# Performance work log

Measured on AMD Instinct MI355X. Metric: run time of the kernel, lower is better.

Reference implementation:

```python
import jax, jax.numpy as jnp
import numpy as np

NUM_EXPERT = 16
IN_FEAT = 1024
OUT_FEAT = 1024
BATCH = 8192


def setup_inputs() -> dict:
    key = jax.random.key(0)
    k_inp, k_gate, k_w = jax.random.split(key, 3)
    inp = jax.random.normal(k_inp, (BATCH, IN_FEAT), dtype=jnp.float32)
    gate = jax.random.randint(k_gate, (BATCH,), 0, NUM_EXPERT, dtype=jnp.int32)
    # nn.Linear default init: uniform(-1/sqrt(in_feat), 1/sqrt(in_feat))
    bound = 1.0 / np.sqrt(IN_FEAT)
    weight = jax.random.uniform(
        k_w, (NUM_EXPERT, OUT_FEAT, IN_FEAT), dtype=jnp.float32,
        minval=-bound, maxval=bound)
    return {"inp": inp, "gate": gate, "weight": weight}


def reference(inp, gate, weight):
    # o[t] = weight[gate[t]] @ inp[t]
    # Loop over the (small, fixed) expert axis via lax.scan; each step does a
    # dense [B, in] @ [in, out] GEMM and keeps rows routed to that expert.
    num_expert, out_feat, _ = weight.shape
    batch = inp.shape[0]

    def body(o, xs):
        i, w = xs  # w: [out_feat, in_feat]
        y = inp @ w.T  # [batch, out_feat]
        sel = (gate == i)[:, None]
        return jnp.where(sel, y, o), None

    o0 = jnp.zeros((batch, out_feat), dtype=inp.dtype)
    o, _ = jax.lax.scan(body, o0, (jnp.arange(num_expert), weight))
    return o
```

## Files before the change

### kernel.cpp

```cpp
#include <hip/hip_runtime.h>
#include <hip/hip_bf16.h>

#define NE    16
#define KDIM  1024
#define NDIM  1024
#define BATCH 8192
#define TM    128
#define TN    64
#define MAXT  96

typedef __attribute__((ext_vector_type(8))) short short8;
typedef __attribute__((ext_vector_type(4))) float floatx4;
typedef unsigned short ushort_t;

#define O_TG0  1024
#define O_TE   2048
#define O_TEND 3072
#define O_GIDX 4096
#define O_TOK  36864
#define O_PA   73728
#define WS_REQ 17113088

#define GLOAD_LDS(gp, lp) __builtin_amdgcn_global_load_lds( \
    (const __attribute__((address_space(1))) unsigned int*)(gp), \
    (__attribute__((address_space(3))) unsigned int*)(lp), 16, 0, 0)

__device__ __forceinline__ unsigned int pk2bf(float x, float y) {
    __hip_bfloat162 h = __float22bfloat162_rn(make_float2(x, y));
    unsigned int u;
    __builtin_memcpy(&u, &h, 4);
    return u;
}


__global__ __launch_bounds__(1024) void map_k(
        const int* __restrict__ gate, int* __restrict__ gidx,
        int* __restrict__ tg0, int* __restrict__ te, int* __restrict__ tend) {
    __shared__ int ccnt[128][NE];
    __shared__ int cbase[128][NE];
    __shared__ int ebase[NE];
    __shared__ int etot[NE];
    const int tid = threadIdx.x;
    const int wv = tid >> 6, ln = tid & 63;

    ((int*)ccnt)[tid] = 0;
    ((int*)ccnt)[tid + 1024] = 0;
    __syncthreads();

    int e[8], rk[8];
    #pragma unroll
    for (int i = 0; i < 8; ++i) {
        const int chunk = wv * 8 + i;
        const int t = chunk * 64 + ln;
        const int ei = gate[t];
        unsigned long long m = ~0ull;
        #pragma unroll
        for (int b = 0; b < 4; ++b) {
            unsigned long long bb = __ballot(((ei >> b) & 1) != 0);
            m &= ((ei >> b) & 1) ? bb : ~bb;
        }
        const unsigned int lo = (unsigned int)m;
        const unsigned int hi = (unsigned int)(m >> 32);
        const int r = __builtin_amdgcn_mbcnt_hi(
            hi, __builtin_amdgcn_mbcnt_lo(lo, 0));
        if (r == 0) ccnt[chunk][ei] = __popcll(m);
        e[i] = ei; rk[i] = r;
    }
    __syncthreads();

    if (tid < NE) {
        int s = 0;
        for (int c = 0; c < 128; ++c) { cbase[c][tid] = s; s += ccnt[c][tid]; }
        etot[tid] = s;
    }
    __syncthreads();

    if (tid == 0) {
        int o = 0, nt = 0;
        for (int j = 0; j < NE; ++j) {
            ebase[j] = o;
            int c = etot[j];
            for (int rr = 0; rr < c; rr += TM) {
                int r0 = (rr + TM <= c) ? rr : (c > TM ? c - TM : 0);
                tg0[nt] = o + r0; te[nt] = j; tend[nt] = o + c; ++nt;
            }
            o += c;
        }
        for (; nt < MAXT; ++nt) { tg0[nt] = 0; te[nt] = 0; tend[nt] = 0; }
    }
    __syncthreads();

    #pragma unroll
    for (int i = 0; i < 8; ++i) {
        const int chunk = wv * 8 + i;
        const int t = chunk * 64 + ln;
        gidx[t] = ebase[e[i]] + cbase[chunk][e[i]] + rk[i];
    }
}

__global__ __launch_bounds__(256, 8) void gather_k(
        const float* __restrict__ inp, const int* __restrict__ gidx,
        ushort_t* __restrict__ pA, int* __restrict__ tok) {
    const int b = blockIdx.x, tid = threadIdx.x;
    const int col = (tid & 127) * 8;
    const int half = tid >> 7;
    int g[2]; float4 v0[2], v1[2];
    #pragma unroll
    for (int p = 0; p < 2; ++p) {
        int t = b * 4 + p * 2 + half;
        g[p] = gidx[t];
        v0[p] = *(const float4*)&inp[(size_t)t * KDIM + col];
        v1[p] = *(const float4*)&inp[(size_t)t * KDIM + col + 4];
    }
    #pragma unroll
    for (int p = 0; p < 2; ++p) {
        uint4 u = make_uint4(pk2bf(v0[p].x, v0[p].y), pk2bf(v0[p].z, v0[p].w),
                             pk2bf(v1[p].x, v1[p].y), pk2bf(v1[p].z, v1[p].w));
        *(uint4*)&pA[(size_t)g[p] * KDIM + col] = u;
        if (col == 0) tok[g[p]] = b * 4 + p * 2 + half;
    }
}

__global__ __launch_bounds__(256, 5) void moe_gemm5_k(
        const ushort_t* __restrict__ pA, const float* __restrict__ wgt,
        const int* __restrict__ tg0, const int* __restrict__ teArr,
        const int* __restrict__ tend, const int* __restrict__ tok,
        float* __restrict__ out) {
    const int id  = blockIdx.x;
    const int y   = (id & 7) + 8 * (id >> 7);
    const int xb  = (id >> 3) & 15;
    const int g0  = tg0[y];
    const int end = tend[y];
    if (g0 >= end) return;
    const int e    = teArr[y];
    const int out0 = xb * TN;

    __shared__ ushort_t As[TM][64];
    __shared__ ushort_t Bs[TN][64];
    __shared__ int tok_s[TM];

    const int tid = threadIdx.x;
    if (tid < TM) tok_s[tid] = tok[g0 + tid];

    const int wave = tid >> 6, lane = tid & 63;
    const int wm = (wave >> 1) * 64;
    const int wn = (wave & 1) * 32;
    const int quad = lane >> 4, l16 = lane & 15;

    const ushort_t* Ab = pA + (size_t)g0 * KDIM;
    const float*    Bw = wgt + ((size_t)e * NDIM + out0) * KDIM;

    floatx4 acc[4][2] = {};
    const int slotw = wave * 64 + lane;

    for (int k0 = 0; k0 < KDIM; k0 += 64) {
        float4 bv[2][2];
        #pragma unroll
        for (int i = 0; i < 2; ++i) {
            int slot = i * 256 + slotw;
            int row = slot >> 3;
            int kc = (slot & 7) ^ (row & 7);
            const float* src = Bw + (size_t)row * KDIM + k0 + kc * 8;
            bv[i][0] = *(const float4*)src;
            bv[i][1] = *(const float4*)(src + 4);
        }
        #pragma unroll
        for (int i = 0; i < 4; ++i) {
            int slot = i * 256 + slotw;
            int row = slot >> 3;
            int kc = (slot & 7) ^ (row & 7);
            GLOAD_LDS(Ab + (size_t)row * KDIM + k0 + kc * 8,
                      (ushort_t*)As + (size_t)(i * 256 + wave * 64) * 8);
        }
        #pragma unroll
        for (int i = 0; i < 2; ++i) {
            int slot = i * 256 + slotw;
            uint4 u = make_uint4(pk2bf(bv[i][0].x, bv[i][0].y),
                                 pk2bf(bv[i][0].z, bv[i][0].w),
                                 pk2bf(bv[i][1].x, bv[i][1].y),
                                 pk2bf(bv[i][1].z, bv[i][1].w));
            *(uint4*)((ushort_t*)Bs + (size_t)slot * 8) = u;
        }
        __syncthreads();
        #pragma unroll
        for (int s = 0; s < 2; ++s) {
            short8 a[4], b[2];
            #pragma unroll
            for (int i = 0; i < 4; ++i) {
                int r = wm + i * 16 + l16;
                a[i] = *(const short8*)&As[r][((s * 4 + quad) ^ (r & 7)) * 8];
            }
            #pragma unroll
            for (int j = 0; j < 2; ++j) {
                int r = wn + j * 16 + l16;
                b[j] = *(const short8*)&Bs[r][((s * 4 + quad) ^ (r & 7)) * 8];
            }
            #pragma unroll
            for (int mi = 0; mi < 4; ++mi)
                #pragma unroll
                for (int nj = 0; nj < 2; ++nj)
                    acc[mi][nj] = __builtin_amdgcn_mfma_f32_16x16x32_bf16(
                        a[mi], b[nj], acc[mi][nj], 0, 0, 0);
        }
        __syncthreads();
    }

    #pragma unroll
    for (int mi = 0; mi < 4; ++mi) {
        #pragma unroll
        for (int r = 0; r < 4; ++r) {
            int lrow = wm + mi * 16 + quad * 4 + r;
            if (g0 + lrow < end) {
                int t = tok_s[lrow];
                float* orow = out + (size_t)t * NDIM + out0 + wn + l16;
                #pragma unroll
                for (int nj = 0; nj < 2; ++nj)
                    orow[nj * 16] = acc[mi][nj][r];
            }
        }
    }
}

#define LDW 20
__global__ void zero_k(int* cnt) {
    if (threadIdx.x < NE) cnt[threadIdx.x] = 0;
}

__global__ void bin_tokens_k(const int* __restrict__ gate, int* cnt, int* idx) {
    int t = blockIdx.x * blockDim.x + threadIdx.x;
    if (t < BATCH) {
        int e = gate[t];
        int p = atomicAdd(&cnt[e], 1);
        idx[e * BATCH + p] = t;
    }
}

__global__ __launch_bounds__(256) void moe_gemm_k(
        const float* __restrict__ inp, const float* __restrict__ wgt,
        const int* __restrict__ cnt, const int* __restrict__ idx,
        float* __restrict__ out) {
    const int e = blockIdx.z;
    const int n_e = cnt[e];
    const int row0 = blockIdx.y * TM;
    if (row0 >= n_e) return;
    const int out0 = blockIdx.x * 128;
    __shared__ unsigned int As[TM * LDW];
    __shared__ unsigned int Bs[TM * LDW];
    __shared__ int tok_s[TM];
    const int tid = threadIdx.x;
    if (tid < TM) {
        int g = row0 + tid;
        tok_s[tid] = (g < n_e) ? idx[e * BATCH + g] : -1;
    }
    const int wave = tid >> 6, lane = tid & 63;
    const int wm = (wave >> 1) * 64, wn = (wave & 1) * 64;
    const int quad = lane >> 4, l16 = lane & 15;
    floatx4 acc[4][4] = {};
    const int cg = (tid & 7) * 4;
    const int rbase = tid >> 3;
    const float* wbase = wgt + (size_t)e * KDIM * NDIM;
    for (int k0 = 0; k0 < KDIM; k0 += 32) {
        __syncthreads();
        #pragma unroll
        for (int p = 0; p < 4; ++p) {
            int row = p * 32 + rbase;
            int t = tok_s[row];
            float4 va = make_float4(0.f, 0.f, 0.f, 0.f);
            if (t >= 0) va = *(const float4*)&inp[(size_t)t * KDIM + k0 + cg];
            As[row * LDW + (cg >> 1)]     = pk2bf(va.x, va.y);
            As[row * LDW + (cg >> 1) + 1] = pk2bf(va.z, va.w);
            float4 vb = *(const float4*)&wbase[(size_t)(out0 + row) * KDIM + k0 + cg];
            Bs[row * LDW + (cg >> 1)]     = pk2bf(vb.x, vb.y);
            Bs[row * LDW + (cg >> 1) + 1] = pk2bf(vb.z, vb.w);
        }
        __syncthreads();
        short8 a[4], b[4];
        #pragma unroll
        for (int i = 0; i < 4; ++i)
            a[i] = *(const short8*)&As[(wm + i * 16 + l16) * LDW + quad * 4];
        #pragma unroll
        for (int i = 0; i < 4; ++i)
            b[i] = *(const short8*)&Bs[(wn + i * 16 + l16) * LDW + quad * 4];
        #pragma unroll
        for (int mi = 0; mi < 4; ++mi)
            #pragma unroll
            for (int ni = 0; ni < 4; ++ni)
                acc[mi][ni] = __builtin_amdgcn_mfma_f32_16x16x32_bf16(
                    a[mi], b[ni], acc[mi][ni], 0, 0, 0);
    }
    #pragma unroll
    for (int mi = 0; mi < 4; ++mi) {
        #pragma unroll
        for (int r = 0; r < 4; ++r) {
            int lrow = wm + mi * 16 + quad * 4 + r;
            int t = tok_s[lrow];
            if (t >= 0) {
                float* orow = out + (size_t)t * NDIM + out0 + wn + l16;
                #pragma unroll
                for (int ni = 0; ni < 4; ++ni)
                    orow[ni * 16] = acc[mi][ni][r];
            }
        }
    }
}

extern "C" void kernel_launch(void* const* d_in, const int* in_sizes, int n_in,
                              void* d_out, int out_size, void* d_ws, size_t ws_size,
                              hipStream_t stream) {
    const float* inp  = (const float*)d_in[0];
    const int*   gate = (const int*)d_in[1];
    const float* wgt  = (const float*)d_in[2];
    float*       out  = (float*)d_out;
    char* w = (char*)d_ws;

    if (ws_size >= WS_REQ) {
        int* tg0  = (int*)(w + O_TG0);
        int* te   = (int*)(w + O_TE);
        int* tend = (int*)(w + O_TEND);
        int* gidx = (int*)(w + O_GIDX);
        int* tok  = (int*)(w + O_TOK);
        ushort_t* pA = (ushort_t*)(w + O_PA);

        map_k<<<1, 1024, 0, stream>>>(gate, gidx, tg0, te, tend);
        gather_k<<<2048, 256, 0, stream>>>(inp, gidx, pA, tok);
        moe_gemm5_k<<<16 * MAXT, 256, 0, stream>>>(pA, wgt, tg0, te, tend, tok, out);
    } else {
        int* cnt = (int*)d_ws;
        int* idx = cnt + NE;
        zero_k<<<1, 64, 0, stream>>>(cnt);
        bin_tokens_k<<<BATCH / 256, 256, 0, stream>>>(gate, cnt, idx);
        dim3 grid(NDIM / 128, BATCH / TM, NE);
        moe_gemm_k<<<grid, 256, 0, stream>>>(inp, wgt, cnt, idx, out);
    }
}
```

Baseline: 180.3 us.

## Fuse token gather and bf16 conversion into the grouped GEMM A-tile load

Drops the separate gather kernel that wrote a permuted bf16 copy of the input. The GEMM now reads fp32 input rows directly through the token index list, converts them to bf16 in registers and stores them to LDS. This saves one kernel launch and a full write and read of the permuted activations. In exchange, each A tile is converted again by every one of the 16 output-column blocks, A traffic is doubled in fp32, and the LDS-direct async loads are gone. The launch also changes to a plain 2D grid without the block-id swizzle, and occupancy drops from 5 to 4 blocks.

```diff
diff --git a/kernel.cpp b/kernel.cpp
--- a/kernel.cpp
+++ b/kernel.cpp
@@ -16,14 +16,8 @@
 #define O_TG0  1024
 #define O_TE   2048
 #define O_TEND 3072
-#define O_GIDX 4096
 #define O_TOK  36864
-#define O_PA   73728
 #define WS_REQ 17113088
-
-#define GLOAD_LDS(gp, lp) __builtin_amdgcn_global_load_lds( \
-    (const __attribute__((address_space(1))) unsigned int*)(gp), \
-    (__attribute__((address_space(3))) unsigned int*)(lp), 16, 0, 0)
 
 __device__ __forceinline__ unsigned int pk2bf(float x, float y) {
     __hip_bfloat162 h = __float22bfloat162_rn(make_float2(x, y));
@@ -34,7 +28,7 @@
 
 
 __global__ __launch_bounds__(1024) void map_k(
-        const int* __restrict__ gate, int* __restrict__ gidx,
+        const int* __restrict__ gate, int* __restrict__ tok,
         int* __restrict__ tg0, int* __restrict__ te, int* __restrict__ tend) {
     __shared__ int ccnt[128][NE];
     __shared__ int cbase[128][NE];
@@ -94,46 +88,22 @@
     for (int i = 0; i < 8; ++i) {
         const int chunk = wv * 8 + i;
         const int t = chunk * 64 + ln;
-        gidx[t] = ebase[e[i]] + cbase[chunk][e[i]] + rk[i];
-    }
-}
-
-__global__ __launch_bounds__(256, 8) void gather_k(
-        const float* __restrict__ inp, const int* __restrict__ gidx,
-        ushort_t* __restrict__ pA, int* __restrict__ tok) {
-    const int b = blockIdx.x, tid = threadIdx.x;
-    const int col = (tid & 127) * 8;
-    const int half = tid >> 7;
-    int g[2]; float4 v0[2], v1[2];
-    #pragma unroll
-    for (int p = 0; p < 2; ++p) {
-        int t = b * 4 + p * 2 + half;
-        g[p] = gidx[t];
-        v0[p] = *(const float4*)&inp[(size_t)t * KDIM + col];
-        v1[p] = *(const float4*)&inp[(size_t)t * KDIM + col + 4];
-    }
-    #pragma unroll
-    for (int p = 0; p < 2; ++p) {
-        uint4 u = make_uint4(pk2bf(v0[p].x, v0[p].y), pk2bf(v0[p].z, v0[p].w),
-                             pk2bf(v1[p].x, v1[p].y), pk2bf(v1[p].z, v1[p].w));
-        *(uint4*)&pA[(size_t)g[p] * KDIM + col] = u;
-        if (col == 0) tok[g[p]] = b * 4 + p * 2 + half;
-    }
-}
-
-__global__ __launch_bounds__(256, 5) void moe_gemm5_k(
-        const ushort_t* __restrict__ pA, const float* __restrict__ wgt,
+        tok[ebase[e[i]] + cbase[chunk][e[i]] + rk[i]] = t;
+    }
+    if (tid < TM) tok[BATCH + tid] = 0;
+}
+
+__global__ __launch_bounds__(256, 4) void moe_gemm6_k(
+        const float* __restrict__ inp, const float* __restrict__ wgt,
         const int* __restrict__ tg0, const int* __restrict__ teArr,
         const int* __restrict__ tend, const int* __restrict__ tok,
         float* __restrict__ out) {
-    const int id  = blockIdx.x;
-    const int y   = (id & 7) + 8 * (id >> 7);
-    const int xb  = (id >> 3) & 15;
+    const int y   = blockIdx.y;
     const int g0  = tg0[y];
     const int end = tend[y];
     if (g0 >= end) return;
     const int e    = teArr[y];
-    const int out0 = xb * TN;
+    const int out0 = blockIdx.x * TN;
 
     __shared__ ushort_t As[TM][64];
     __shared__ ushort_t Bs[TN][64];
@@ -147,39 +117,51 @@
     const int wn = (wave & 1) * 32;
     const int quad = lane >> 4, l16 = lane & 15;
 
-    const ushort_t* Ab = pA + (size_t)g0 * KDIM;
-    const float*    Bw = wgt + ((size_t)e * NDIM + out0) * KDIM;
+    const int rbase = tid >> 3;
+    const int dcol  = (tid & 7) * 8;
+    const int kc    = ((tid & 7) ^ (rbase & 7)) * 8;
+
+    __syncthreads();
+
+    const float* arow[4];
+    #pragma unroll
+    for (int i = 0; i < 4; ++i)
+        arow[i] = inp + (size_t)tok_s[rbase + 32 * i] * KDIM + kc;
+    const float* Bw = wgt + ((size_t)e * NDIM + out0) * KDIM;
+    const float* brow[2];
+    #pragma unroll
+    for (int i = 0; i < 2; ++i)
+        brow[i] = Bw + (size_t)(rbase + 32 * i) * KDIM + kc;
 
     floatx4 acc[4][2] = {};
-    const int slotw = wave * 64 + lane;
 
     for (int k0 = 0; k0 < KDIM; k0 += 64) {
-        float4 bv[2][2];
+        float4 av[4][2], bv[2][2];
+        #pragma unroll
+        for (int i = 0; i < 4; ++i) {
+            av[i][0] = *(const float4*)(arow[i] + k0);
+            av[i][1] = *(const float4*)(arow[i] + k0 + 4);
+        }
         #pragma unroll
         for (int i = 0; i < 2; ++i) {
-            int slot = i * 256 + slotw;
-            int row = slot >> 3;
-            int kc = (slot & 7) ^ (row & 7);
-            const float* src = Bw + (size_t)row * KDIM + k0 + kc * 8;
-            bv[i][0] = *(const float4*)src;
-            bv[i][1] = *(const float4*)(src + 4);
+            bv[i][0] = *(const float4*)(brow[i] + k0);
+            bv[i][1] = *(const float4*)(brow[i] + k0 + 4);
         }
         #pragma unroll
         for (int i = 0; i < 4; ++i) {
-            int slot = i * 256 + slotw;
-            int row = slot >> 3;
-            int kc = (slot & 7) ^ (row & 7);
-            GLOAD_LDS(Ab + (size_t)row * KDIM + k0 + kc * 8,
-                      (ushort_t*)As + (size_t)(i * 256 + wave * 64) * 8);
+            uint4 u = make_uint4(pk2bf(av[i][0].x, av[i][0].y),
+                                 pk2bf(av[i][0].z, av[i][0].w),
+                                 pk2bf(av[i][1].x, av[i][1].y),
+                                 pk2bf(av[i][1].z, av[i][1].w));
+            *(uint4*)&As[rbase + 32 * i][dcol] = u;
         }
         #pragma unroll
         for (int i = 0; i < 2; ++i) {
-            int slot = i * 256 + slotw;
             uint4 u = make_uint4(pk2bf(bv[i][0].x, bv[i][0].y),
                                  pk2bf(bv[i][0].z, bv[i][0].w),
                                  pk2bf(bv[i][1].x, bv[i][1].y),
                                  pk2bf(bv[i][1].z, bv[i][1].w));
-            *(uint4*)((ushort_t*)Bs + (size_t)slot * 8) = u;
+            *(uint4*)&Bs[rbase + 32 * i][dcol] = u;
         }
         __syncthreads();
         #pragma unroll
@@ -317,13 +299,11 @@
         int* tg0  = (int*)(w + O_TG0);
         int* te   = (int*)(w + O_TE);
         int* tend = (int*)(w + O_TEND);
-        int* gidx = (int*)(w + O_GIDX);
         int* tok  = (int*)(w + O_TOK);
-        ushort_t* pA = (ushort_t*)(w + O_PA);
-
-        map_k<<<1, 1024, 0, stream>>>(gate, gidx, tg0, te, tend);
-        gather_k<<<2048, 256, 0, stream>>>(inp, gidx, pA, tok);
-        moe_gemm5_k<<<16 * MAXT, 256, 0, stream>>>(pA, wgt, tg0, te, tend, tok, out);
+
+        map_k<<<1, 1024, 0, stream>>>(gate, tok, tg0, te, tend);
+        dim3 grid(NDIM / TN, MAXT, 1);
+        moe_gemm6_k<<<grid, 256, 0, stream>>>(inp, wgt, tg0, te, tend, tok, out);
     } else {
         int* cnt = (int*)d_ws;
         int* idx = cnt + NE;
```

Measured after the change: 209.4 us. +16.1%, slower.

## Register-prefetch next K tile in MoE GEMM, replace LDS-direct A loads

Applied to the files above, without the earlier changes.

The grouped GEMM now loads the next K-slice of A and B into registers right after the barrier, so global latency overlaps with the MFMA work on the current slice. The A loads change from global_load_lds to ordinary register loads followed by LDS stores. The trailing barrier becomes a manual lgkmcnt wait plus s_barrier so outstanding vector-memory prefetches are not drained. The grid changes from a 1D swizzled mapping to a plain 2D grid, and occupancy hints drop from 5 to 4 blocks per CU, since holding the prefetch in registers raises register pressure and may reduce occupancy and L2 locality.

```diff
diff --git a/kernel.cpp b/kernel.cpp
--- a/kernel.cpp
+++ b/kernel.cpp
@@ -20,10 +20,6 @@
 #define O_TOK  36864
 #define O_PA   73728
 #define WS_REQ 17113088
-
-#define GLOAD_LDS(gp, lp) __builtin_amdgcn_global_load_lds( \
-    (const __attribute__((address_space(1))) unsigned int*)(gp), \
-    (__attribute__((address_space(3))) unsigned int*)(lp), 16, 0, 0)
 
 __device__ __forceinline__ unsigned int pk2bf(float x, float y) {
     __hip_bfloat162 h = __float22bfloat162_rn(make_float2(x, y));
@@ -121,19 +117,17 @@
     }
 }
 
-__global__ __launch_bounds__(256, 5) void moe_gemm5_k(
+__global__ __launch_bounds__(256, 4) void moe_gemm8_k(
         const ushort_t* __restrict__ pA, const float* __restrict__ wgt,
         const int* __restrict__ tg0, const int* __restrict__ teArr,
         const int* __restrict__ tend, const int* __restrict__ tok,
         float* __restrict__ out) {
-    const int id  = blockIdx.x;
-    const int y   = (id & 7) + 8 * (id >> 7);
-    const int xb  = (id >> 3) & 15;
+    const int y   = blockIdx.y;
     const int g0  = tg0[y];
     const int end = tend[y];
     if (g0 >= end) return;
     const int e    = teArr[y];
-    const int out0 = xb * TN;
+    const int out0 = blockIdx.x * TN;
 
     __shared__ ushort_t As[TM][64];
     __shared__ ushort_t Bs[TN][64];
@@ -146,35 +140,45 @@
     const int wm = (wave >> 1) * 64;
     const int wn = (wave & 1) * 32;
     const int quad = lane >> 4, l16 = lane & 15;
+    const int c8 = tid & 7;
+    const int rb = tid >> 3;
 
     const ushort_t* Ab = pA + (size_t)g0 * KDIM;
     const float*    Bw = wgt + ((size_t)e * NDIM + out0) * KDIM;
 
+    const ushort_t* asrc[4];
+    #pragma unroll
+    for (int i = 0; i < 4; ++i) {
+        int row = rb + 32 * i;
+        asrc[i] = Ab + (size_t)row * KDIM + (c8 ^ (row & 7)) * 8;
+    }
+    const float* bsrc[2];
+    #pragma unroll
+    for (int i = 0; i < 2; ++i) {
+        int slot = i * 256 + tid;
+        int row = slot >> 3;
+        bsrc[i] = Bw + (size_t)row * KDIM + ((slot & 7) ^ (row & 7)) * 8;
+    }
+
     floatx4 acc[4][2] = {};
-    const int slotw = wave * 64 + lane;
+    uint4  av[4];
+    float4 bv[2][2];
+
+    #pragma unroll
+    for (int i = 0; i < 4; ++i) av[i] = *(const uint4*)(asrc[i]);
+    #pragma unroll
+    for (int i = 0; i < 2; ++i) {
+        bv[i][0] = *(const float4*)(bsrc[i]);
+        bv[i][1] = *(const float4*)(bsrc[i] + 4);
+    }
 
     for (int k0 = 0; k0 < KDIM; k0 += 64) {
-        float4 bv[2][2];
+        #pragma unroll
+        for (int i = 0; i < 4; ++i)
+            *(uint4*)&As[rb + 32 * i][c8 * 8] = av[i];
         #pragma unroll
         for (int i = 0; i < 2; ++i) {
-            int slot = i * 256 + slotw;
-            int row = slot >> 3;
-            int kc = (slot & 7) ^ (row & 7);
-            const float* src = Bw + (size_t)row * KDIM + k0 + kc * 8;
-            bv[i][0] = *(const float4*)src;
-            bv[i][1] = *(const float4*)(src + 4);
-        }
-        #pragma unroll
-        for (int i = 0; i < 4; ++i) {
-            int slot = i * 256 + slotw;
-            int row = slot >> 3;
-            int kc = (slot & 7) ^ (row & 7);
-            GLOAD_LDS(Ab + (size_t)row * KDIM + k0 + kc * 8,
-                      (ushort_t*)As + (size_t)(i * 256 + wave * 64) * 8);
-        }
-        #pragma unroll
-        for (int i = 0; i < 2; ++i) {
-            int slot = i * 256 + slotw;
+            int slot = i * 256 + tid;
             uint4 u = make_uint4(pk2bf(bv[i][0].x, bv[i][0].y),
                                  pk2bf(bv[i][0].z, bv[i][0].w),
                                  pk2bf(bv[i][1].x, bv[i][1].y),
@@ -182,6 +186,18 @@
             *(uint4*)((ushort_t*)Bs + (size_t)slot * 8) = u;
         }
         __syncthreads();
+
+        if (k0 + 64 < KDIM) {
+            #pragma unroll
+            for (int i = 0; i < 4; ++i)
+                av[i] = *(const uint4*)(asrc[i] + k0 + 64);
+            #pragma unroll
+            for (int i = 0; i < 2; ++i) {
+                bv[i][0] = *(const float4*)(bsrc[i] + k0 + 64);
+                bv[i][1] = *(const float4*)(bsrc[i] + k0 + 68);
+            }
+        }
+
         #pragma unroll
         for (int s = 0; s < 2; ++s) {
             short8 a[4], b[2];
@@ -202,7 +218,8 @@
                     acc[mi][nj] = __builtin_amdgcn_mfma_f32_16x16x32_bf16(
                         a[mi], b[nj], acc[mi][nj], 0, 0, 0);
         }
-        __syncthreads();
+        asm volatile("s_waitcnt lgkmcnt(0)" ::: "memory");
+        __builtin_amdgcn_s_barrier();
     }
 
     #pragma unroll
@@ -323,7 +340,8 @@
 
         map_k<<<1, 1024, 0, stream>>>(gate, gidx, tg0, te, tend);
         gather_k<<<2048, 256, 0, stream>>>(inp, gidx, pA, tok);
-        moe_gemm5_k<<<16 * MAXT, 256, 0, stream>>>(pA, wgt, tg0, te, tend, tok, out);
+        dim3 grid(NDIM / TN, MAXT, 1);
+        moe_gemm8_k<<<grid, 256, 0, stream>>>(pA, wgt, tg0, te, tend, tok, out);
     } else {
         int* cnt = (int*)d_ws;
         int* idx = cnt + NE;
```

Result: slower. 252.4 us (+40.0%).
